# Kernel tuning notes

Hardware: AMD Instinct MI355X
Metric: run time of the kernel (lower is better)

## Reference

```python
import jax, jax.numpy as jnp
import numpy as np

B, C, H, W = 4, 32, 64, 64
K = 3
HEADS = 8
SF = 4
D = C * K * K          # 288, unfold token dim
E = D // 2             # 144, reduced dim
DH = E // HEADS        # 18, head dim
SCALE = DH ** -0.5
N = H * W              # 4096 tokens


def unfold(x):
    # x: (B,C,H,W) -> (B, C*K*K, H*W), torch.nn.Unfold ordering (c, kh, kw)
    xp = jnp.pad(x, ((0, 0), (0, 0), (1, 1), (1, 1)))
    patches = jnp.stack([xp[:, :, i:i + H, j:j + W] for i in range(K) for j in range(K)], axis=2)
    return patches.reshape(x.shape[0], C * K * K, H * W)


def fold(cols):
    # inverse of unfold: scatter-add overlapping patches back, crop padding
    b = cols.shape[0]
    y = cols.reshape(b, C, K, K, H, W)
    out = jnp.zeros((b, C, H + 2, W + 2), cols.dtype)
    for i in range(K):
        for j in range(K):
            out = out.at[:, :, i:i + H, j:j + W].add(y[:, :, i, j])
    return out[:, :, 1:-1, 1:-1]


def layernorm_cols(cols, g, b):
    # LayerNorm over D applied on (B,N,D) view, returned as (B,D,N)
    xt = cols.transpose(0, 2, 1)
    mu = xt.mean(-1, keepdims=True)
    var = xt.var(-1, keepdims=True)
    y = (xt - mu) / jnp.sqrt(var + 1e-5) * g + b
    return y.transpose(0, 2, 1)


def emha(x, wr, br, wqkv, we, be):
    # x: (B, D, N)
    b, _, n_tok = x.shape
    xr = jnp.einsum('bdn,ed->ben', x, wr) + br[None, :, None]   # Conv1d k=1 reduction
    t = xr.transpose(0, 2, 1)                                   # (B,N,E)
    qkv = t @ wqkv.T                                            # Linear, no bias
    q, k, v = jnp.split(qkv, 3, axis=-1)
    n = n_tok // SF

    def rs(a):
        return a.reshape(b, n_tok, HEADS, DH).transpose(0, 2, 1, 3).reshape(b, HEADS, SF, n, DH)

    q, k, v = rs(q), rs(k), rs(v)
    attn = jax.nn.softmax(jnp.einsum('bhsnd,bhsmd->bhsnm', q, k) * SCALE, axis=-1)
    o = jnp.einsum('bhsnm,bhsmd->bhsnd', attn, v)
    o = o.reshape(b, HEADS, n_tok, DH).transpose(0, 2, 1, 3).reshape(b, n_tok, E).transpose(0, 2, 1)
    return jnp.einsum('ben,fe->bfn', o, we) + be[None, :, None]  # Conv1d k=1 expansion


def conv3x3(x, w, b):
    y = jax.lax.conv_general_dilated(x, w, (1, 1), ((1, 1), (1, 1)),
                                     dimension_numbers=('NCHW', 'OIHW', 'NCHW'))
    return y + b[None, :, None, None]


def setup_inputs() -> dict:
    key = jax.random.key(0)
    ks = jax.random.split(key, 20)
    s = 0.02
    inp = {
        'x': jax.random.normal(ks[0], (B, C, H, W), jnp.float32),
        'ln_g': jnp.ones((D,), jnp.float32),
        'ln_b': jnp.zeros((D,), jnp.float32),
        'conv_w': jax.random.normal(ks[1], (C, C, 3, 3), jnp.float32) * s,
        'conv_b': jnp.zeros((C,), jnp.float32),
    }
    for i in range(3):
        k0, k1, k2 = jax.random.split(ks[2 + i], 3)
        inp[f'wr{i+1}'] = jax.random.normal(k0, (E, D), jnp.float32) * s
        inp[f'br{i+1}'] = jnp.zeros((E,), jnp.float32)
        inp[f'wqkv{i+1}'] = jax.random.normal(k1, (3 * E, E), jnp.float32) * s
        inp[f'we{i+1}'] = jax.random.normal(k2, (D, E), jnp.float32) * s
        inp[f'be{i+1}'] = jnp.zeros((D,), jnp.float32)
    return inp


def reference(x, ln_g, ln_b, conv_w, conv_b,
              wr1, br1, wqkv1, we1, be1,
              wr2, br2, wqkv2, we2, be2,
              wr3, br3, wqkv3, we3, be3):
    t = x
    for (wr, br, wqkv, we, be) in ((wr1, br1, wqkv1, we1, be1),
                                   (wr2, br2, wqkv2, we2, be2),
                                   (wr3, br3, wqkv3, we3, be3)):
        cols = unfold(t)
        cols_n = layernorm_cols(cols, ln_g, ln_b)
        cols = emha(cols_n, wr, br, wqkv, we, be) + cols
        t = fold(cols)
    return x + jax.nn.elu(conv3x3(t, conv_w, conv_b))
```

## Files before the change

kernel.cpp:

```cpp
#include <hip/hip_runtime.h>
#include <math.h>

#define BN 4
#define CC 32
#define HH 64
#define WW 64
#define DD 288
#define EE 144
#define NTOK 4096
#define SCALE_F 0.2357022603955158f
#define QSCALE  0.3401074286f
#define QST 192
#define KST 32
#define MQKV 528

typedef __bf16 bf16x8 __attribute__((ext_vector_type(8)));
typedef float floatx4 __attribute__((ext_vector_type(4)));
typedef unsigned short u16x8 __attribute__((ext_vector_type(8)));

__device__ __forceinline__ unsigned short f2bf(float x) {
    unsigned int u = __float_as_uint(x);
    u += 0x7fffu + ((u >> 16) & 1u);
    return (unsigned short)(u >> 16);
}
__device__ __forceinline__ float bf2f(unsigned short s) {
    return __uint_as_float(((unsigned int)s) << 16);
}
__device__ __forceinline__ unsigned int pack_bf_trunc(float a, float b) {
    return __builtin_amdgcn_perm(__float_as_uint(b), __float_as_uint(a), 0x07060302u);
}
__device__ __forceinline__ void plswap32(unsigned int& a, unsigned int& b) {
    asm("v_permlane32_swap_b32 %0, %1" : "+v"(a), "+v"(b));
}
__device__ __forceinline__ void plswap16(unsigned int& a, unsigned int& b) {
    asm("v_permlane16_swap_b32 %0, %1" : "+v"(a), "+v"(b));
}

__global__ __launch_bounds__(256) void setup_k(
    const float* __restrict__ wr0, const float* __restrict__ br0,
    const float* __restrict__ wr1, const float* __restrict__ br1,
    const float* __restrict__ wr2, const float* __restrict__ br2,
    const float* __restrict__ g,  const float* __restrict__ lb,
    const float* __restrict__ wqkv0, const float* __restrict__ wqkv1, const float* __restrict__ wqkv2,
    const float* __restrict__ we0,   const float* __restrict__ we1,   const float* __restrict__ we2,
    unsigned short* __restrict__ wg_bf, float* __restrict__ wgsum, float* __restrict__ wbeta,
    unsigned short* __restrict__ wqkv_bf, unsigned short* __restrict__ we_bf)
{
    int blk = blockIdx.x;
    int tid = threadIdx.x;
    if (blk < 3) {
        if (tid < 144) {
            int l = blk, e = tid;
            const float* wr = (l == 0) ? wr0 : ((l == 1) ? wr1 : wr2);
            const float* br = (l == 0) ? br0 : ((l == 1) ? br1 : br2);
            float sg = 0.f, sb = 0.f;
            for (int d = 0; d < DD; ++d) {
                float w = wr[e * DD + d];
                float wgv = w * g[d];
                wg_bf[((size_t)l * EE + e) * DD + d] = f2bf(wgv);
                sg += wgv;
                sb += w * lb[d];
            }
            wgsum[l * EE + e] = sg;
            wbeta[l * EE + e] = sb + br[e];
        }
        return;
    }
    int idx = (blk - 3) * 256 + tid;
    const int T1 = 3 * MQKV * 160;
    const int T2 = 3 * 288 * 160;
    if (idx < T1) {
        int l = idx / (MQKV * 160), r = idx % (MQKV * 160);
        int m = r / 160, k = r % 160;
        const float* w = (l == 0) ? wqkv0 : ((l == 1) ? wqkv1 : wqkv2);
        float v = 0.f;
        if (k < 144) {
            if (m < 192) {
                int h = m / 24, j = m % 24;
                if (j < 18) v = w[(h * 18 + j) * 144 + k] * QSCALE;
            } else if (m < 384) {
                int mm = m - 192, h = mm / 24, j = mm % 24;
                if (j < 18) v = w[(144 + h * 18 + j) * 144 + k];
            } else {
                v = w[(288 + (m - 384)) * 144 + k];
            }
        }
        wqkv_bf[idx] = f2bf(v);
    } else if (idx < T1 + T2) {
        int j = idx - T1;
        int l = j / (288 * 160), r = j % (288 * 160);
        int m = r / 160, k = r % 160;
        const float* w = (l == 0) ? we0 : ((l == 1) ? we1 : we2);
        we_bf[j] = (k < 144) ? f2bf(w[m * 144 + k]) : 0;
    }
}

__global__ __launch_bounds__(256) void unfold_k(const float* __restrict__ t,
    unsigned short* __restrict__ colsT,
    float* __restrict__ mu, float* __restrict__ rstd)
{
    __shared__ float red1[4][64], red2[4][64];
    int tid = threadIdx.x;
    int lane = tid & 63, cpart = tid >> 6;
    int b = blockIdx.x >> 6, nc = blockIdx.x & 63;
    int n = nc * 64 + lane;
    int h = n >> 6, w = n & 63;
    const float* tb = t + (size_t)b * CC * HH * WW;
    unsigned short loc[72];
    float s1 = 0.f, s2 = 0.f;
    #pragma unroll
    for (int c8 = 0; c8 < 8; ++c8) {
        int c = cpart * 8 + c8;
        const float* tc = tb + (size_t)c * 4096;
        #pragma unroll
        for (int i = 0; i < 3; ++i) {
            int hr = h + i - 1;
            bool rok = ((unsigned)hr < 64u);
            #pragma unroll
            for (int j = 0; j < 3; ++j) {
                int wc = w + j - 1;
                bool ok = rok && ((unsigned)wc < 64u);
                float v = ok ? tc[hr * 64 + wc] : 0.f;
                loc[c8 * 9 + i * 3 + j] = f2bf(v);
                s1 += v;
                s2 = fmaf(v, v, s2);
            }
        }
    }
    unsigned short* ct = colsT + ((size_t)b * NTOK + n) * 288 + cpart * 72;
    #pragma unroll
    for (int u = 0; u < 9; ++u)
        *(u16x8*)&ct[u * 8] = *(const u16x8*)&loc[u * 8];
    red1[cpart][lane] = s1;
    red2[cpart][lane] = s2;
    __syncthreads();
    if (tid < 64) {
        float a = red1[0][tid] + red1[1][tid] + red1[2][tid] + red1[3][tid];
        float q = red2[0][tid] + red2[1][tid] + red2[2][tid] + red2[3][tid];
        float m = a * (1.f / 288.f);
        float var = q * (1.f / 288.f) - m * m;
        int nn = nc * 64 + tid;
        mu[b * NTOK + nn] = m;
        rstd[b * NTOK + nn] = rsqrtf(var + 1e-5f);
    }
}

template<int K, int MODE, int NYB>
__global__ __launch_bounds__(256) void mgemm_k(
    const unsigned short* __restrict__ A, const unsigned short* __restrict__ Bt, int BST,
    unsigned short* __restrict__ Ct, unsigned short* __restrict__ Cv, unsigned short* __restrict__ Ck,
    const float* __restrict__ mu, const float* __restrict__ rstd,
    const float* __restrict__ wgsum, const float* __restrict__ wbeta,
    const float* __restrict__ bias)
{
    constexpr int NT = 64;
    __shared__ unsigned short Ts[64 * 56];
    int flat = blockIdx.x;
    int g  = (flat / (8 * NYB)) * 8 + (flat & 7);
    int jm = (flat % (8 * NYB)) >> 3;
    int n0 = (g & 63) * NT;
    int bI = g >> 6;
    int m0 = jm * 48;
    int tid = threadIdx.x;
    int wv = tid >> 6, lane = tid & 63;
    int l15 = lane & 15, l4 = lane >> 4;

    const unsigned short* Arow = A + (size_t)(m0 + l15) * K + l4 * 8;
    const unsigned short* Brow = Bt + ((size_t)bI * NTOK + n0 + wv * 16 + l15) * BST + l4 * 8;

    floatx4 acc[3];
    acc[0] = acc[1] = acc[2] = (floatx4){0.f, 0.f, 0.f, 0.f};

    #pragma unroll
    for (int ks = 0; ks < K / 32; ++ks) {
        bf16x8 bfr = *(const bf16x8*)(Brow + ks * 32);
        #pragma unroll
        for (int mi = 0; mi < 3; ++mi) {
            bf16x8 af = *(const bf16x8*)(Arow + (size_t)mi * 16 * K + ks * 32);
            acc[mi] = __builtin_amdgcn_mfma_f32_16x16x32_bf16(af, bfr, acc[mi], 0, 0, 0);
        }
    }

    int n_l = wv * 16 + l15;

    if (MODE == 2) {
        #pragma unroll
        for (int mi = 0; mi < 3; ++mi)
            #pragma unroll
            for (int r = 0; r < 4; ++r) {
                int m_l = mi * 16 + l4 * 4 + r;
                Ts[m_l * 72 + n_l] = f2bf(acc[mi][r] + bias[m0 + m_l]);
            }
        __syncthreads();
        for (int u = tid; u < 48 * 8; u += 256) {
            int row = u >> 3, seg = u & 7;
            unsigned short* dst = Ct + ((size_t)bI * DD + m0 + row) * NTOK + n0 + seg * 8;
            *(u16x8*)dst = *(const u16x8*)&Ts[row * 72 + seg * 8];
        }
    } else {
        bool vpath = (MODE == 0) && (m0 >= 384);
        float muv = 0.f, rsv = 0.f;
        if (MODE == 1) {
            int n_g = n0 + n_l;
            muv = mu[bI * NTOK + n_g];
            rsv = rstd[bI * NTOK + n_g];
        }
        #pragma unroll
        for (int mi = 0; mi < 3; ++mi)
            #pragma unroll
            for (int r = 0; r < 4; ++r) {
                int m_l = mi * 16 + l4 * 4 + r;
                float v = acc[mi][r];
                if (MODE == 1) v = rsv * (v - muv * wgsum[m0 + m_l]) + wbeta[m0 + m_l];
                if (!vpath) Ts[n_l * 56 + m_l] = f2bf(v);
                else        Ts[m_l * 72 + n_l] = f2bf(v);
            }
        __syncthreads();
        if (!vpath) {
            if (tid < 128) {
                int row = tid >> 1, half = tid & 1;
                const unsigned short* src = &Ts[row * 56 + half * 24];
                if (MODE == 0 && m0 >= 192) {
                    int head = (m0 - 192) / 24 + half;
                    unsigned short* dst = Ck + ((size_t)(bI * 8 + head) * NTOK + n0 + row) * KST;
                    #pragma unroll
                    for (int u = 0; u < 3; ++u)
                        *(u16x8*)&dst[u * 8] = *(const u16x8*)&src[u * 8];
                    *(u16x8*)&dst[24] = (u16x8)0;
                } else {
                    const int CTS = (MODE == 1) ? 160 : QST;
                    unsigned short* dst = Ct + ((size_t)bI * NTOK + n0 + row) * CTS + m0 + half * 24;
                    #pragma unroll
                    for (int u = 0; u < 3; ++u)
                        *(u16x8*)&dst[u * 8] = *(const u16x8*)&src[u * 8];
                    if (MODE == 1 && m0 == 96) {
                        u16x8 z = (u16x8)0;
                        *(u16x8*)(Ct + ((size_t)bI * NTOK + n0 + row) * 160 + 144 + half * 8) = z;
                    }
                }
            }
        } else {
            for (int u = tid; u < 48 * 8; u += 256) {
                int row = u >> 3, seg = u & 7;
                unsigned short* dst = Cv + ((size_t)bI * EE + (m0 - 384) + row) * NTOK + n0 + seg * 8;
                *(u16x8*)dst = *(const u16x8*)&Ts[row * 72 + seg * 8];
            }
        }
    }
}

__global__ __launch_bounds__(256, 4) void attn_k2(const unsigned short* __restrict__ qT,
                                                  const unsigned short* __restrict__ kP,
                                                  const unsigned short* __restrict__ vF,
                                                  unsigned short* __restrict__ oT)
{
    __shared__ unsigned short Vs[32 * 136];

    int blk = blockIdx.x;
    int bhs = blk & 127;
    int qc  = blk >> 7;
    int b = bhs >> 5, h = (bhs >> 2) & 7, s = bhs & 3;
    int tid  = threadIdx.x;
    int wv   = tid >> 6;
    int lane = tid & 63;
    int l15 = lane & 15, l4 = lane >> 4;
    int q0 = qc * 64;
    int tokbase = s * 1024;

    for (int v = tid; v < 14 * 16; v += 256) {
        int d = 18 + (v >> 4), seg = v & 15;
        unsigned short val = (d == 31) ? (unsigned short)0x3F80 : (unsigned short)0;
        u16x8 vv = (u16x8)val;
        *(u16x8*)&Vs[d * 136 + seg * 8] = vv;
    }

    bf16x8 qf;
    {
        u16x8 raw = *(const u16x8*)(qT + ((size_t)b * NTOK + tokbase + q0 + wv * 16 + l15) * QST
                                    + 24 * h + l4 * 8);
        if (l4 == 3) raw = (u16x8)0;
        qf = *(bf16x8*)&raw;
    }

    floatx4 oacc[2];
    oacc[0] = (floatx4){0.f, 0.f, 0.f, 0.f};
    oacc[1] = (floatx4){0.f, 0.f, 0.f, 0.f};

    const unsigned short* vbb = vF + (size_t)b * EE * NTOK + tokbase;
    int d0 = tid >> 4, seg0 = tid & 15;
    bool x2 = (tid < 32);
    int d1 = 16 + (tid >> 4), seg1 = tid & 15;
    u16x8 pv0, pv1;
    pv0 = *(const u16x8*)(vbb + (size_t)(h * 18 + d0) * NTOK + seg0 * 8);
    if (x2) pv1 = *(const u16x8*)(vbb + (size_t)(h * 18 + d1) * NTOK + seg1 * 8);

    const unsigned short* kRow = kP + ((size_t)(b * 8 + h) * NTOK + tokbase + l15) * KST + l4 * 8;

    for (int c0 = 0; c0 < 1024; c0 += 128) {
        bf16x8 kreg[8];
        #pragma unroll
        for (int sub = 0; sub < 2; ++sub)
            #pragma unroll
            for (int mi = 0; mi < 4; ++mi) {
                u16x8 raw = *(const u16x8*)(kRow + (unsigned)(c0 + sub * 64 + mi * 16) * KST);
                kreg[sub * 4 + mi] = *(bf16x8*)&raw;
            }

        __syncthreads();
        *(u16x8*)&Vs[d0 * 136 + seg0 * 8] = pv0;
        if (x2) *(u16x8*)&Vs[d1 * 136 + seg1 * 8] = pv1;
        int cn = c0 + 128;
        if (cn < 1024) {
            pv0 = *(const u16x8*)(vbb + (size_t)(h * 18 + d0) * NTOK + cn + seg0 * 8);
            if (x2) pv1 = *(const u16x8*)(vbb + (size_t)(h * 18 + d1) * NTOK + cn + seg1 * 8);
        }
        __syncthreads();

        #pragma unroll
        for (int sub = 0; sub < 2; ++sub) {
            floatx4 sacc[4];
            #pragma unroll
            for (int mi = 0; mi < 4; ++mi) {
                floatx4 z = (floatx4){0.f, 0.f, 0.f, 0.f};
                sacc[mi] = __builtin_amdgcn_mfma_f32_16x16x32_bf16(kreg[sub * 4 + mi], qf, z, 0, 0, 0);
            }

            unsigned int pk0[4], pk1[4];
            #pragma unroll
            for (int mi = 0; mi < 4; ++mi) {
                pk0[mi] = pack_bf_trunc(__builtin_amdgcn_exp2f(sacc[mi][0]),
                                        __builtin_amdgcn_exp2f(sacc[mi][1]));
                pk1[mi] = pack_bf_trunc(__builtin_amdgcn_exp2f(sacc[mi][2]),
                                        __builtin_amdgcn_exp2f(sacc[mi][3]));
            }

            #pragma unroll
            for (int c = 0; c < 2; ++c) {
                unsigned int B0 = pk0[2 * c], B2 = pk0[2 * c + 1];
                unsigned int B1 = pk1[2 * c], B3 = pk1[2 * c + 1];
                plswap32(B0, B2); plswap16(B0, B2);
                plswap32(B1, B3); plswap16(B1, B3);
                union { unsigned int u[4]; bf16x8 v; } bfr;
                bfr.u[0] = B0; bfr.u[1] = B1; bfr.u[2] = B2; bfr.u[3] = B3;
                #pragma unroll
                for (int nd = 0; nd < 2; ++nd) {
                    bf16x8 af = *(const bf16x8*)&Vs[(nd * 16 + l15) * 136 + sub * 64 + c * 32 + l4 * 8];
                    oacc[nd] = __builtin_amdgcn_mfma_f32_16x16x32_bf16(af, bfr.v, oacc[nd], 0, 0, 0);
                }
            }
        }
    }

    float lsum = __shfl(oacc[1][3], 48 + l15, 64);
    float inv  = 1.f / lsum;
    size_t rowi = (size_t)b * NTOK + tokbase + q0 + wv * 16 + l15;
    unsigned short* orow = oT + rowi * 160 + h * 18;
    unsigned int w0 = (unsigned)f2bf(oacc[0][0] * inv) | ((unsigned)f2bf(oacc[0][1] * inv) << 16);
    unsigned int w1 = (unsigned)f2bf(oacc[0][2] * inv) | ((unsigned)f2bf(oacc[0][3] * inv) << 16);
    *(unsigned int*)&orow[l4 * 4]     = w0;
    *(unsigned int*)&orow[l4 * 4 + 2] = w1;
    if (l4 == 0) {
        unsigned int w2 = (unsigned)f2bf(oacc[1][0] * inv) | ((unsigned)f2bf(oacc[1][1] * inv) << 16);
        *(unsigned int*)&orow[16] = w2;
    }
    if (h == 7 && l4 < 2) {
        u16x8 z = (u16x8)0;
        *(u16x8*)(oT + rowi * 160 + 144 + l4 * 8) = z;
    }
}

__global__ __launch_bounds__(256) void fold_k(const unsigned short* __restrict__ cols,
                                              const float* __restrict__ tprev,
                                              float* __restrict__ t)
{
    int idx = blockIdx.x * 256 + threadIdx.x;
    int w = idx & 63;
    int h = (idx >> 6) & 63;
    int c = (idx >> 12) & 31;
    int b = idx >> 17;
    const unsigned short* cb = cols + (size_t)b * DD * NTOK + (size_t)c * 9 * NTOK;
    float sum = 0.f;
    #pragma unroll
    for (int i = 0; i < 3; ++i) {
        int hs = h + 1 - i;
        if ((unsigned)hs < 64u) {
            #pragma unroll
            for (int j = 0; j < 3; ++j) {
                int ws_ = w + 1 - j;
                if ((unsigned)ws_ < 64u)
                    sum += bf2f(cb[(size_t)(i * 3 + j) * NTOK + hs * 64 + ws_]);
            }
        }
    }
    int ch = (h == 0 || h == 63) ? 2 : 3;
    int cw_ = (w == 0 || w == 63) ? 2 : 3;
    t[idx] = sum + (float)(ch * cw_) * tprev[idx];
}

__global__ __launch_bounds__(256) void conv_k(const float* __restrict__ t,
    const float* __restrict__ cw, const float* __restrict__ cbias,
    const float* __restrict__ x, float* __restrict__ out)
{
    __shared__ float wsh[CC * 9];
    int blk = blockIdx.x;
    int band = blk & 3, co = (blk >> 2) & 31, b = blk >> 7;
    int tid = threadIdx.x;
    for (int u = tid; u < CC * 9; u += 256) wsh[u] = cw[co * CC * 9 + u];
    __syncthreads();
    int h = band * 16 + (tid >> 4);
    int w0 = (tid & 15) << 2;
    const float* tb = t + (size_t)b * CC * 4096;
    float bias = cbias[co];
    float a0 = bias, a1 = bias, a2 = bias, a3 = bias;
    for (int ci = 0; ci < CC; ++ci) {
        const float* tc = tb + (size_t)ci * 4096;
        const float* wr = &wsh[ci * 9];
        #pragma unroll
        for (int i = 0; i < 3; ++i) {
            int hr = h + i - 1;
            if ((unsigned)hr < 64u) {
                const float* row = tc + hr * 64;
                float vl = (w0 > 0)  ? row[w0 - 1] : 0.f;
                float4 c4 = *(const float4*)&row[w0];
                float vr = (w0 < 60) ? row[w0 + 4] : 0.f;
                float wj0 = wr[i * 3], wj1 = wr[i * 3 + 1], wj2 = wr[i * 3 + 2];
                a0 = fmaf(wj0, vl,   a0); a0 = fmaf(wj1, c4.x, a0); a0 = fmaf(wj2, c4.y, a0);
                a1 = fmaf(wj0, c4.x, a1); a1 = fmaf(wj1, c4.y, a1); a1 = fmaf(wj2, c4.z, a1);
                a2 = fmaf(wj0, c4.y, a2); a2 = fmaf(wj1, c4.z, a2); a2 = fmaf(wj2, c4.w, a2);
                a3 = fmaf(wj0, c4.z, a3); a3 = fmaf(wj1, c4.w, a3); a3 = fmaf(wj2, vr,   a3);
            }
        }
    }
    size_t oidx = ((size_t)(b * CC + co) * 4096) + h * 64 + w0;
    float4 xin = *(const float4*)&x[oidx];
    float4 o;
    o.x = xin.x + ((a0 > 0.f) ? a0 : (__expf(a0) - 1.f));
    o.y = xin.y + ((a1 > 0.f) ? a1 : (__expf(a1) - 1.f));
    o.z = xin.z + ((a2 > 0.f) ? a2 : (__expf(a2) - 1.f));
    o.w = xin.w + ((a3 > 0.f) ? a3 : (__expf(a3) - 1.f));
    *(float4*)&out[oidx] = o;
}

extern "C" void kernel_launch(void* const* d_in, const int* in_sizes, int n_in,
                              void* d_out, int out_size, void* d_ws, size_t ws_size,
                              hipStream_t stream)
{
    const float* x    = (const float*)d_in[0];
    const float* ln_g = (const float*)d_in[1];
    const float* ln_b = (const float*)d_in[2];
    const float* cw   = (const float*)d_in[3];
    const float* cb   = (const float*)d_in[4];
    const float* wr[3]   = {(const float*)d_in[5],  (const float*)d_in[10], (const float*)d_in[15]};
    const float* br[3]   = {(const float*)d_in[6],  (const float*)d_in[11], (const float*)d_in[16]};
    const float* wqkv[3] = {(const float*)d_in[7],  (const float*)d_in[12], (const float*)d_in[17]};
    const float* we[3]   = {(const float*)d_in[8],  (const float*)d_in[13], (const float*)d_in[18]};
    const float* be[3]   = {(const float*)d_in[9],  (const float*)d_in[14], (const float*)d_in[19]};
    float* out = (float*)d_out;

    char* p = (char*)d_ws;
    unsigned short* cols_bf = (unsigned short*)p; p += (size_t)BN * DD * NTOK * 2;
    unsigned short* colsT = (unsigned short*)p; p += (size_t)BN * NTOK * 288 * 2;
    unsigned short* oT = colsT;
    unsigned short* xrT   = (unsigned short*)p; p += (size_t)BN * NTOK * 160 * 2;
    unsigned short* qT    = (unsigned short*)p; p += (size_t)BN * NTOK * QST * 2;
    unsigned short* kP    = (unsigned short*)p; p += (size_t)BN * 8 * NTOK * KST * 2;
    unsigned short* vF    = (unsigned short*)p; p += (size_t)BN * EE * NTOK * 2;
    float* mu   = (float*)p;              p += (size_t)BN * NTOK * 4;
    float* rstd = (float*)p;              p += (size_t)BN * NTOK * 4;
    float* tA   = (float*)p;              p += (size_t)BN * CC * HH * WW * 4;
    float* tB   = (float*)p;              p += (size_t)BN * CC * HH * WW * 4;
    unsigned short* wg_bf   = (unsigned short*)p; p += (size_t)3 * EE * DD * 2;
    unsigned short* wqkv_bf = (unsigned short*)p; p += (size_t)3 * MQKV * 160 * 2;
    unsigned short* we_bf   = (unsigned short*)p; p += (size_t)3 * DD * 160 * 2;
    float* wgsum = (float*)p;             p += 3 * EE * 4;
    float* wbeta = (float*)p;             p += 3 * EE * 4;
    (void)in_sizes; (void)n_in; (void)out_size; (void)ws_size;

    setup_k<<<1533, 256, 0, stream>>>(wr[0], br[0], wr[1], br[1], wr[2], br[2], ln_g, ln_b,
                                      wqkv[0], wqkv[1], wqkv[2], we[0], we[1], we[2],
                                      wg_bf, wgsum, wbeta, wqkv_bf, we_bf);

    const float* tin = x;
    float* touts[3] = {tA, tB, tA};
    for (int l = 0; l < 3; ++l) {
        unfold_k<<<256, 256, 0, stream>>>(tin, colsT, mu, rstd);
        mgemm_k<288, 1, 3><<<768, 256, 0, stream>>>(
            wg_bf + (size_t)l * EE * DD, colsT, 288, xrT, nullptr, nullptr,
            mu, rstd, wgsum + l * EE, wbeta + l * EE, nullptr);
        mgemm_k<160, 0, 11><<<2816, 256, 0, stream>>>(
            wqkv_bf + (size_t)l * MQKV * 160, xrT, 160, qT, vF, kP,
            nullptr, nullptr, nullptr, nullptr, nullptr);
        attn_k2<<<2048, 256, 0, stream>>>(qT, kP, vF, oT);
        mgemm_k<160, 2, 6><<<1536, 256, 0, stream>>>(
            we_bf + (size_t)l * DD * 160, oT, 160, cols_bf, nullptr, nullptr,
            nullptr, nullptr, nullptr, nullptr, be[l]);
        fold_k<<<2048, 256, 0, stream>>>(cols_bf, tin, touts[l]);
        tin = touts[l];
    }
    conv_k<<<512, 256, 0, stream>>>(tA, cw, cb, x, out);
}
```

Before: 420.7 us.

## Fuse unfold, layernorm stats and reduction GEMM; switch PV MFMA to 16x16x16

Merges the unfold kernel and the first reduction GEMM into one kernel that builds the unfolded tile in shared memory, computes layernorm statistics there, and runs the MFMA GEMM directly from LDS. This removes the colsT and mu/rstd global round trips and one kernel launch per layer. The attention PV product also moves from the 16x16x32 MFMA with permlane swaps to the 16x16x16 variant, which needs no lane shuffles but issues twice as many MFMAs. The fused kernel uses 512 threads per block and a large LDS footprint, but only 256 blocks.

```diff
diff --git a/kernel.cpp b/kernel.cpp
--- a/kernel.cpp
+++ b/kernel.cpp
@@ -17,6 +17,7 @@
 typedef __bf16 bf16x8 __attribute__((ext_vector_type(8)));
 typedef float floatx4 __attribute__((ext_vector_type(4)));
 typedef unsigned short u16x8 __attribute__((ext_vector_type(8)));
+typedef short s16x4 __attribute__((ext_vector_type(4)));
 
 __device__ __forceinline__ unsigned short f2bf(float x) {
     unsigned int u = __float_as_uint(x);
@@ -28,12 +29,6 @@
 }
 __device__ __forceinline__ unsigned int pack_bf_trunc(float a, float b) {
     return __builtin_amdgcn_perm(__float_as_uint(b), __float_as_uint(a), 0x07060302u);
-}
-__device__ __forceinline__ void plswap32(unsigned int& a, unsigned int& b) {
-    asm("v_permlane32_swap_b32 %0, %1" : "+v"(a), "+v"(b));
-}
-__device__ __forceinline__ void plswap16(unsigned int& a, unsigned int& b) {
-    asm("v_permlane16_swap_b32 %0, %1" : "+v"(a), "+v"(b));
 }
 
 __global__ __launch_bounds__(256) void setup_k(
@@ -95,53 +90,100 @@
     }
 }
 
-__global__ __launch_bounds__(256) void unfold_k(const float* __restrict__ t,
-    unsigned short* __restrict__ colsT,
-    float* __restrict__ mu, float* __restrict__ rstd)
-{
-    __shared__ float red1[4][64], red2[4][64];
+__global__ __launch_bounds__(512) void fgemm1_k(
+    const float* __restrict__ t, const unsigned short* __restrict__ wg,
+    const float* __restrict__ wgsum, const float* __restrict__ wbeta,
+    unsigned short* __restrict__ xrT)
+{
+    __shared__ unsigned short Cs[64 * 296];
+    __shared__ float red1[8][64], red2[8][64];
     int tid = threadIdx.x;
-    int lane = tid & 63, cpart = tid >> 6;
+    int lane = tid & 63, part = tid >> 6;
     int b = blockIdx.x >> 6, nc = blockIdx.x & 63;
-    int n = nc * 64 + lane;
-    int h = n >> 6, w = n & 63;
+    int w = lane;
     const float* tb = t + (size_t)b * CC * HH * WW;
-    unsigned short loc[72];
+    __attribute__((aligned(8))) unsigned short loc[36];
     float s1 = 0.f, s2 = 0.f;
     #pragma unroll
-    for (int c8 = 0; c8 < 8; ++c8) {
-        int c = cpart * 8 + c8;
+    for (int c4 = 0; c4 < 4; ++c4) {
+        int c = part * 4 + c4;
         const float* tc = tb + (size_t)c * 4096;
         #pragma unroll
         for (int i = 0; i < 3; ++i) {
-            int hr = h + i - 1;
+            int hr = nc + i - 1;
             bool rok = ((unsigned)hr < 64u);
             #pragma unroll
             for (int j = 0; j < 3; ++j) {
                 int wc = w + j - 1;
                 bool ok = rok && ((unsigned)wc < 64u);
                 float v = ok ? tc[hr * 64 + wc] : 0.f;
-                loc[c8 * 9 + i * 3 + j] = f2bf(v);
+                loc[c4 * 9 + i * 3 + j] = f2bf(v);
                 s1 += v;
                 s2 = fmaf(v, v, s2);
             }
         }
     }
-    unsigned short* ct = colsT + ((size_t)b * NTOK + n) * 288 + cpart * 72;
-    #pragma unroll
-    for (int u = 0; u < 9; ++u)
-        *(u16x8*)&ct[u * 8] = *(const u16x8*)&loc[u * 8];
-    red1[cpart][lane] = s1;
-    red2[cpart][lane] = s2;
+    {
+        unsigned short* cr = &Cs[lane * 296 + part * 36];
+        #pragma unroll
+        for (int k = 0; k < 9; ++k)
+            *(unsigned long long*)&cr[k * 4] = *(const unsigned long long*)&loc[k * 4];
+    }
+    red1[part][lane] = s1;
+    red2[part][lane] = s2;
     __syncthreads();
     if (tid < 64) {
-        float a = red1[0][tid] + red1[1][tid] + red1[2][tid] + red1[3][tid];
-        float q = red2[0][tid] + red2[1][tid] + red2[2][tid] + red2[3][tid];
+        float a = 0.f, q = 0.f;
+        #pragma unroll
+        for (int p = 0; p < 8; ++p) { a += red1[p][tid]; q += red2[p][tid]; }
         float m = a * (1.f / 288.f);
         float var = q * (1.f / 288.f) - m * m;
-        int nn = nc * 64 + tid;
-        mu[b * NTOK + nn] = m;
-        rstd[b * NTOK + nn] = rsqrtf(var + 1e-5f);
+        red1[0][tid] = m;
+        red2[0][tid] = rsqrtf(var + 1e-5f);
+    }
+    __syncthreads();
+
+    int l15 = lane & 15, l4 = lane >> 4;
+    int tw = part & 3, mh = part >> 2;
+    const unsigned short* Ar = wg + (size_t)(mh * 16 + l15) * DD + l4 * 8;
+    floatx4 acc[5];
+    #pragma unroll
+    for (int i = 0; i < 5; ++i) acc[i] = (floatx4){0.f, 0.f, 0.f, 0.f};
+    #pragma unroll
+    for (int ks = 0; ks < 9; ++ks) {
+        bf16x8 bfr = *(const bf16x8*)&Cs[(tw * 16 + l15) * 296 + ks * 32 + l4 * 8];
+        #pragma unroll
+        for (int i = 0; i < 4; ++i) {
+            bf16x8 af = *(const bf16x8*)(Ar + (size_t)i * 32 * DD + ks * 32);
+            acc[i] = __builtin_amdgcn_mfma_f32_16x16x32_bf16(af, bfr, acc[i], 0, 0, 0);
+        }
+        if (mh == 0) {
+            bf16x8 af = *(const bf16x8*)(Ar + (size_t)4 * 32 * DD + ks * 32);
+            acc[4] = __builtin_amdgcn_mfma_f32_16x16x32_bf16(af, bfr, acc[4], 0, 0, 0);
+        }
+    }
+
+    __syncthreads();
+    {
+        int tok = tw * 16 + l15;
+        float muv = red1[0][tok], rsv = red2[0][tok];
+        #pragma unroll
+        for (int i = 0; i < 5; ++i) {
+            if (i == 4 && mh) break;
+            #pragma unroll
+            for (int r = 0; r < 4; ++r) {
+                int m = (mh + 2 * i) * 16 + l4 * 4 + r;
+                float v = rsv * (acc[i][r] - muv * wgsum[m]) + wbeta[m];
+                Cs[tok * 296 + m] = f2bf(v);
+            }
+        }
+    }
+    __syncthreads();
+    for (int u = tid; u < 64 * 20; u += 512) {
+        int row = u / 20, seg = u - row * 20;
+        unsigned short* dst = xrT + ((size_t)b * NTOK + nc * 64 + row) * 160 + seg * 8;
+        u16x8 val = (seg < 18) ? *(const u16x8*)&Cs[row * 296 + seg * 8] : (u16x8)0;
+        *(u16x8*)dst = val;
     }
 }
 
@@ -149,8 +191,6 @@
 __global__ __launch_bounds__(256) void mgemm_k(
     const unsigned short* __restrict__ A, const unsigned short* __restrict__ Bt, int BST,
     unsigned short* __restrict__ Ct, unsigned short* __restrict__ Cv, unsigned short* __restrict__ Ck,
-    const float* __restrict__ mu, const float* __restrict__ rstd,
-    const float* __restrict__ wgsum, const float* __restrict__ wbeta,
     const float* __restrict__ bias)
 {
     constexpr int NT = 64;
@@ -198,20 +238,13 @@
             *(u16x8*)dst = *(const u16x8*)&Ts[row * 72 + seg * 8];
         }
     } else {
-        bool vpath = (MODE == 0) && (m0 >= 384);
-        float muv = 0.f, rsv = 0.f;
-        if (MODE == 1) {
-            int n_g = n0 + n_l;
-            muv = mu[bI * NTOK + n_g];
-            rsv = rstd[bI * NTOK + n_g];
-        }
+        bool vpath = (m0 >= 384);
         #pragma unroll
         for (int mi = 0; mi < 3; ++mi)
             #pragma unroll
             for (int r = 0; r < 4; ++r) {
                 int m_l = mi * 16 + l4 * 4 + r;
                 float v = acc[mi][r];
-                if (MODE == 1) v = rsv * (v - muv * wgsum[m0 + m_l]) + wbeta[m0 + m_l];
                 if (!vpath) Ts[n_l * 56 + m_l] = f2bf(v);
                 else        Ts[m_l * 72 + n_l] = f2bf(v);
             }
@@ -220,7 +253,7 @@
             if (tid < 128) {
                 int row = tid >> 1, half = tid & 1;
                 const unsigned short* src = &Ts[row * 56 + half * 24];
-                if (MODE == 0 && m0 >= 192) {
+                if (m0 >= 192) {
                     int head = (m0 - 192) / 24 + half;
                     unsigned short* dst = Ck + ((size_t)(bI * 8 + head) * NTOK + n0 + row) * KST;
                     #pragma unroll
@@ -228,15 +261,10 @@
                         *(u16x8*)&dst[u * 8] = *(const u16x8*)&src[u * 8];
                     *(u16x8*)&dst[24] = (u16x8)0;
                 } else {
-                    const int CTS = (MODE == 1) ? 160 : QST;
-                    unsigned short* dst = Ct + ((size_t)bI * NTOK + n0 + row) * CTS + m0 + half * 24;
+                    unsigned short* dst = Ct + ((size_t)bI * NTOK + n0 + row) * QST + m0 + half * 24;
                     #pragma unroll
                     for (int u = 0; u < 3; ++u)
                         *(u16x8*)&dst[u * 8] = *(const u16x8*)&src[u * 8];
-                    if (MODE == 1 && m0 == 96) {
-                        u16x8 z = (u16x8)0;
-                        *(u16x8*)(Ct + ((size_t)bI * NTOK + n0 + row) * 160 + 144 + half * 8) = z;
-                    }
                 }
             }
         } else {
@@ -328,24 +356,18 @@
             unsigned int pk0[4], pk1[4];
             #pragma unroll
             for (int mi = 0; mi < 4; ++mi) {
-                pk0[mi] = pack_bf_trunc(__builtin_amdgcn_exp2f(sacc[mi][0]),
-                                        __builtin_amdgcn_exp2f(sacc[mi][1]));
-                pk1[mi] = pack_bf_trunc(__builtin_amdgcn_exp2f(sacc[mi][2]),
-                                        __builtin_amdgcn_exp2f(sacc[mi][3]));
-            }
-
-            #pragma unroll
-            for (int c = 0; c < 2; ++c) {
-                unsigned int B0 = pk0[2 * c], B2 = pk0[2 * c + 1];
-                unsigned int B1 = pk1[2 * c], B3 = pk1[2 * c + 1];
-                plswap32(B0, B2); plswap16(B0, B2);
-                plswap32(B1, B3); plswap16(B1, B3);
-                union { unsigned int u[4]; bf16x8 v; } bfr;
-                bfr.u[0] = B0; bfr.u[1] = B1; bfr.u[2] = B2; bfr.u[3] = B3;
+                pk0[mi] = pack_bf_trunc(exp2f(sacc[mi][0]), exp2f(sacc[mi][1]));
+                pk1[mi] = pack_bf_trunc(exp2f(sacc[mi][2]), exp2f(sacc[mi][3]));
+            }
+
+            #pragma unroll
+            for (int tt = 0; tt < 4; ++tt) {
+                union { unsigned int u[2]; s16x4 v; } pb;
+                pb.u[0] = pk0[tt]; pb.u[1] = pk1[tt];
                 #pragma unroll
                 for (int nd = 0; nd < 2; ++nd) {
-                    bf16x8 af = *(const bf16x8*)&Vs[(nd * 16 + l15) * 136 + sub * 64 + c * 32 + l4 * 8];
-                    oacc[nd] = __builtin_amdgcn_mfma_f32_16x16x32_bf16(af, bfr.v, oacc[nd], 0, 0, 0);
+                    s16x4 af = *(const s16x4*)&Vs[(nd * 16 + l15) * 136 + sub * 64 + tt * 16 + l4 * 4];
+                    oacc[nd] = __builtin_amdgcn_mfma_f32_16x16x16bf16_1k(af, pb.v, oacc[nd], 0, 0, 0);
                 }
             }
         }
@@ -459,14 +481,11 @@
 
     char* p = (char*)d_ws;
     unsigned short* cols_bf = (unsigned short*)p; p += (size_t)BN * DD * NTOK * 2;
-    unsigned short* colsT = (unsigned short*)p; p += (size_t)BN * NTOK * 288 * 2;
-    unsigned short* oT = colsT;
+    unsigned short* oT    = (unsigned short*)p; p += (size_t)BN * NTOK * 288 * 2;
     unsigned short* xrT   = (unsigned short*)p; p += (size_t)BN * NTOK * 160 * 2;
     unsigned short* qT    = (unsigned short*)p; p += (size_t)BN * NTOK * QST * 2;
     unsigned short* kP    = (unsigned short*)p; p += (size_t)BN * 8 * NTOK * KST * 2;
     unsigned short* vF    = (unsigned short*)p; p += (size_t)BN * EE * NTOK * 2;
-    float* mu   = (float*)p;              p += (size_t)BN * NTOK * 4;
-    float* rstd = (float*)p;              p += (size_t)BN * NTOK * 4;
     float* tA   = (float*)p;              p += (size_t)BN * CC * HH * WW * 4;
     float* tB   = (float*)p;              p += (size_t)BN * CC * HH * WW * 4;
     unsigned short* wg_bf   = (unsigned short*)p; p += (size_t)3 * EE * DD * 2;
@@ -483,17 +502,13 @@
     const float* tin = x;
     float* touts[3] = {tA, tB, tA};
     for (int l = 0; l < 3; ++l) {
-        unfold_k<<<256, 256, 0, stream>>>(tin, colsT, mu, rstd);
-        mgemm_k<288, 1, 3><<<768, 256, 0, stream>>>(
-            wg_bf + (size_t)l * EE * DD, colsT, 288, xrT, nullptr, nullptr,
-            mu, rstd, wgsum + l * EE, wbeta + l * EE, nullptr);
+        fgemm1_k<<<256, 512, 0, stream>>>(tin, wg_bf + (size_t)l * EE * DD,
+                                          wgsum + l * EE, wbeta + l * EE, xrT);
         mgemm_k<160, 0, 11><<<2816, 256, 0, stream>>>(
-            wqkv_bf + (size_t)l * MQKV * 160, xrT, 160, qT, vF, kP,
-            nullptr, nullptr, nullptr, nullptr, nullptr);
+            wqkv_bf + (size_t)l * MQKV * 160, xrT, 160, qT, vF, kP, nullptr);
         attn_k2<<<2048, 256, 0, stream>>>(qT, kP, vF, oT);
         mgemm_k<160, 2, 6><<<1536, 256, 0, stream>>>(
-            we_bf + (size_t)l * DD * 160, oT, 160, cols_bf, nullptr, nullptr,
-            nullptr, nullptr, nullptr, nullptr, be[l]);
+            we_bf + (size_t)l * DD * 160, oT, 160, cols_bf, nullptr, nullptr, be[l]);
         fold_k<<<2048, 256, 0, stream>>>(cols_bf, tin, touts[l]);
         tin = touts[l];
     }
```

After: 420.7 us. Within noise of the previous version (+0.0%).
